# Performance work log

Hardware: AMD Instinct MI355X
Metric: run time of the kernel (lower is better)

Reference implementation:

```python
import jax, jax.numpy as jnp
import numpy as np
from jax import lax

THRESHOLD = 0.7
OUT = 224  # output size of nn.Upsample(size=(224,224), mode='bilinear', align_corners=True)


def _bilinear(img, xs, ys):
    """align_corners=True bilinear sampling. img: (..., H, W); xs: (oh,), ys: (ow,) float coords."""
    H, W = img.shape[-2], img.shape[-1]
    x0 = jnp.clip(jnp.floor(xs).astype(jnp.int32), 0, H - 1)
    x1 = jnp.clip(x0 + 1, 0, H - 1)
    y0 = jnp.clip(jnp.floor(ys).astype(jnp.int32), 0, W - 1)
    y1 = jnp.clip(y0 + 1, 0, W - 1)
    wx = (xs - x0.astype(xs.dtype))[:, None]  # (oh,1)
    wy = (ys - y0.astype(ys.dtype))[None, :]  # (1,ow)
    top = jnp.take(img, x0, axis=-2)
    bot = jnp.take(img, x1, axis=-2)
    v00 = jnp.take(top, y0, axis=-1)
    v01 = jnp.take(top, y1, axis=-1)
    v10 = jnp.take(bot, y0, axis=-1)
    v11 = jnp.take(bot, y1, axis=-1)
    return (1 - wx) * ((1 - wy) * v00 + wy * v01) + wx * ((1 - wy) * v10 + wy * v11)


def _normalize01(h):
    n = h.shape[0]
    f = h.reshape(n, -1)
    mn = f.min(axis=1, keepdims=True)
    mx = f.max(axis=1, keepdims=True)
    return ((f - mn) / (mx - mn)).reshape(h.shape)


def _largest_cc(mask):
    """8-connected (skimage connectivity=2) largest component via min-label propagation.
    mask: (N,H,W) bool -> (N,H,W) bool, True on the largest connected component."""
    N, H, W = mask.shape
    BIG = H * W  # background sentinel label
    idx = jnp.arange(BIG, dtype=jnp.int32).reshape(1, H, W)
    lab0 = jnp.where(mask, idx, BIG)

    def body(state):
        lab, _ = state
        pooled = lax.reduce_window(lab, jnp.int32(BIG), lax.min, (1, 3, 3), (1, 1, 1), 'SAME')
        new = jnp.where(mask, pooled, BIG)
        return new, jnp.any(new != lab)

    lab, _ = lax.while_loop(lambda s: s[1], body, (lab0, jnp.bool_(True)))

    def counts(l):
        return jnp.zeros(BIG + 1, jnp.int32).at[l.reshape(-1)].add(1)

    c = jax.vmap(counts)(lab)                 # (N, H*W+1); last bin = background
    best = jnp.argmax(c[:, :BIG], axis=1)     # label of largest foreground component
    return lab == best[:, None, None]


def _bbox(lcc):
    N, H, W = lcc.shape
    rows = lcc.any(axis=2)
    cols = lcc.any(axis=1)
    has = rows.any(axis=1)
    xmin = jnp.argmax(rows, axis=1).astype(jnp.int32)
    xmax = (H - 1 - jnp.argmax(rows[:, ::-1], axis=1)).astype(jnp.int32)
    ymin = jnp.argmax(cols, axis=1).astype(jnp.int32)
    ymax = (W - 1 - jnp.argmax(cols[:, ::-1], axis=1)).astype(jnp.int32)
    # fallback to full image if the mask is empty (torch code would crash here)
    xmin = jnp.where(has, xmin, 0)
    ymin = jnp.where(has, ymin, 0)
    xmax = jnp.where(has, xmax, H - 1)
    ymax = jnp.where(has, ymax, W - 1)
    return xmin, xmax, ymin, ymax


def _crop_resize(images, xmin, xmax, ymin, ymax):
    # torch crop is images[i][:, xmin:xmax, ymin:ymax] (exclusive upper), then align_corners resize
    grid = jnp.arange(OUT, dtype=jnp.float32) / (OUT - 1)

    def one(img, a, b, c, d):
        Lx = jnp.maximum(b - a, 1)
        Ly = jnp.maximum(d - c, 1)
        xs = a.astype(jnp.float32) + grid * (Lx - 1).astype(jnp.float32)
        ys = c.astype(jnp.float32) + grid * (Ly - 1).astype(jnp.float32)
        return _bilinear(img, xs, ys)

    return jax.vmap(one)(images, xmin, xmax, ymin, ymax)


def setup_inputs() -> dict:
    key = jax.random.key(0)
    k1, k2 = jax.random.split(key)
    x = jax.random.normal(k1, (64, 3, 224, 224), dtype=jnp.float32)
    features = jax.random.normal(k2, (64, 2048, 7, 7), dtype=jnp.float32)
    return {"x": x, "features": features}


def reference(x, features):
    # distance = normalize01(Lmax(features, axis=1))
    heat = _normalize01(jnp.max(jnp.abs(features), axis=1))       # (N, h, w)
    h, w = heat.shape[1], heat.shape[2]
    grid = jnp.arange(OUT, dtype=jnp.float32) / (OUT - 1)
    out_heatmap = _bilinear(heat, grid * (h - 1), grid * (w - 1))  # (N, 224, 224)
    mask = out_heatmap > THRESHOLD
    lcc = _largest_cc(mask)
    xmin, xmax, ymin, ymax = _bbox(lcc)
    crop = _crop_resize(x, xmin, xmax, ymin, ymax)                 # (N, 3, 224, 224)
    coords = jnp.stack([ymin, xmin, ymax, xmax], axis=1)           # (N, 4), torch coord order
    return crop, out_heatmap, coords
```

## Files before the change

kernel.cpp:

```cpp
#include <hip/hip_runtime.h>
#include <stdint.h>

#define NIMG   64
#define NCH    2048
#define HW7    49
#define OUTW   224
#define NPIX   50176
#define CROP_N 9633792
#define HEAT_OFF  9633792
#define COORD_OFF 12845056
#define THRESH 0.7f

#define MAXR 4
#define RCAP (224*MAXR)
#define NWORDS 784
#define WPAD   788

#define NGRP 16


__global__ __launch_bounds__(256) void k1_heat(const float* __restrict__ F,
                                               float* __restrict__ heatPart) {
    __shared__ float smax[4][64];
    const int t = threadIdx.x;
    const int b = blockIdx.x;
    const int n = b >> 4, g = b & 15;
    const int w = t >> 6, l = t & 63;
    const int lp = (l < HW7) ? l : 0;
    const float* base = F + (size_t)n * 100352 + (size_t)(g * 128 + w) * HW7 + lp;
    float vmax = 0.0f;
#pragma unroll 8
    for (int i = 0; i < 32; ++i) {
        vmax = fmaxf(vmax, fabsf(base[(size_t)i * 4 * HW7]));
    }
    smax[w][l] = vmax;
    __syncthreads();
    if (t < HW7) {
        float m = fmaxf(fmaxf(smax[0][t], smax[1][t]), fmaxf(smax[2][t], smax[3][t]));
        heatPart[b * HW7 + t] = m;
    }
}

__device__ inline unsigned uf_find(volatile unsigned* P, unsigned x) {
    while (true) {
        unsigned p = P[x];
        if (p == x) return x;
        unsigned gp = P[p];
        if (gp == p) return p;
        P[x] = gp;
        x = gp;
    }
}

__device__ inline void uf_merge(volatile unsigned* P, unsigned a, unsigned b) {
    while (true) {
        a = uf_find(P, a); b = uf_find(P, b);
        if (a == b) return;
        if (a > b) { unsigned tmp = a; a = b; b = tmp; }
        unsigned old = atomicCAS((unsigned*)&P[b], b, a);
        if (old == b) return;
        b = old;
    }
}

__global__ __launch_bounds__(1024) void k23_heat_ccl(const float* __restrict__ heatPart,
                                                     float* __restrict__ heatOut,
                                                     float* __restrict__ coords) {
#pragma clang fp contract(off)
    __shared__ float raw[HW7];
    __shared__ float h7[HW7];
    __shared__ float s_mn, s_mx;
    __shared__ float wT[OUTW];
    __shared__ int   i0T[OUTW];
    __shared__ int   i1T[OUTW];
    __shared__ unsigned long long W[WPAD];
    __shared__ unsigned short runS[RCAP], runE[RCAP];
    __shared__ unsigned char nRuns[224];
    __shared__ unsigned parent[RCAP], cnt[RCAP];
    __shared__ unsigned rmin[RCAP], rmax[RCAP], cmin[RCAP], cmax[RCAP];
    __shared__ unsigned bestScore, bestRid;

    const int t = threadIdx.x;
    const int n = blockIdx.x;

    if (t < HW7) {
        float m = heatPart[(n * NGRP + 0) * HW7 + t];
#pragma unroll
        for (int g = 1; g < NGRP; ++g) m = fmaxf(m, heatPart[(n * NGRP + g) * HW7 + t]);
        raw[t] = m;
    }
    if (t < OUTW) {
        float gx = (float)t / 223.0f;
        float xs = gx * 6.0f;
        int x0 = (int)floorf(xs); x0 = min(max(x0, 0), 6);
        i0T[t] = x0;
        i1T[t] = min(x0 + 1, 6);
        wT[t]  = xs - (float)x0;
    }
    if (t < RCAP) {
        parent[t] = (unsigned)t; cnt[t] = 0u;
        rmin[t] = 0xFFFFFFFFu; rmax[t] = 0u; cmin[t] = 0xFFFFFFFFu; cmax[t] = 0u;
    }
    if (t >= NWORDS && t < WPAD) W[t] = 0ull;
    if (t == 0) { bestScore = 0u; bestRid = 0u; }
    __syncthreads();
    if (t == 0) {
        float mn = raw[0], mx = raw[0];
        for (int i = 1; i < HW7; ++i) { float v = raw[i]; mn = fminf(mn, v); mx = fmaxf(mx, v); }
        s_mn = mn; s_mx = mx;
    }
    __syncthreads();
    if (t < HW7) h7[t] = (raw[t] - s_mn) / (s_mx - s_mn);
    __syncthreads();

    for (int k = 0; k < 49; ++k) {
        int p = (k << 10) + t;
        int i = p / 224, j = p - i * 224;
        int x0 = i0T[i], x1 = i1T[i];
        int y0 = i0T[j], y1 = i1T[j];
        float wx = wT[i], wy = wT[j];
        float v00 = h7[x0 * 7 + y0], v01 = h7[x0 * 7 + y1];
        float v10 = h7[x1 * 7 + y0], v11 = h7[x1 * 7 + y1];
        float val = (1.0f - wx) * ((1.0f - wy) * v00 + wy * v01)
                  + wx * ((1.0f - wy) * v10 + wy * v11);
        heatOut[(size_t)n * NPIX + p] = val;
        unsigned long long bal = __ballot(val > THRESH);
        if ((t & 63) == 0) W[p >> 6] = bal;
    }
    __syncthreads();

    if (t < 224) {
        const int r = t;
        const int bit0 = r * 224;
        const int w0 = bit0 >> 6, sh = bit0 & 63;
        unsigned long long rb[4];
#pragma unroll
        for (int q = 0; q < 4; ++q) {
            unsigned long long lo = W[w0 + q] >> sh;
            unsigned long long hi = sh ? (W[w0 + q + 1] << (64 - sh)) : 0ull;
            rb[q] = lo | hi;
        }
        rb[3] &= 0xFFFFFFFFull;

        unsigned long long st[4], en[4];
        unsigned long long carry = 0ull;
#pragma unroll
        for (int q = 0; q < 4; ++q) {
            unsigned long long shl = (rb[q] << 1) | carry;
            carry = rb[q] >> 63;
            st[q] = rb[q] & ~shl;
        }
#pragma unroll
        for (int q = 0; q < 4; ++q) {
            unsigned long long nxt = (q < 3) ? rb[q + 1] : 0ull;
            en[q] = rb[q] & ~((rb[q] >> 1) | (nxt << 63));
        }
        int ns = 0;
#pragma unroll
        for (int q = 0; q < 4; ++q) {
            unsigned long long x = st[q];
            while (x) {
                int z = __builtin_ctzll(x); x &= x - 1;
                if (ns < MAXR) runS[r * MAXR + ns] = (unsigned short)(q * 64 + z);
                ns++;
            }
        }
        int ne = 0;
#pragma unroll
        for (int q = 0; q < 4; ++q) {
            unsigned long long x = en[q];
            while (x) {
                int z = __builtin_ctzll(x); x &= x - 1;
                if (ne < MAXR) runE[r * MAXR + ne] = (unsigned short)(q * 64 + z);
                ne++;
            }
        }
        nRuns[r] = (unsigned char)min(ns, MAXR);
    }
    __syncthreads();

    if (t >= MAXR && t < RCAP) {
        const int r = t >> 2, k = t & (MAXR - 1);
        if (k < (int)nRuns[r]) {
            const int nb = nRuns[r - 1];
            int s = runS[t], e = runE[t];
            for (int m = 0; m < nb; ++m) {
                int qid = (r - 1) * MAXR + m;
                int s2 = runS[qid], e2 = runE[qid];
                if (s2 <= e + 1 && e2 >= s - 1) uf_merge(parent, (unsigned)t, (unsigned)qid);
            }
        }
    }
    __syncthreads();

    if (t < RCAP) {
        int r = t >> 2, k = t & (MAXR - 1);
        if (k < (int)nRuns[r]) {
            int s = runS[t], e = runE[t];
            unsigned root = uf_find(parent, (unsigned)t);
            atomicAdd(&cnt[root], (unsigned)(e - s + 1));
            atomicMin(&rmin[root], (unsigned)r);
            atomicMax(&rmax[root], (unsigned)r);
            atomicMin(&cmin[root], (unsigned)s);
            atomicMax(&cmax[root], (unsigned)e);
        }
    }
    __syncthreads();

    if (t < RCAP) {
        unsigned c = cnt[t];
        if (c > 0u) {
            unsigned label = (unsigned)((t >> 2) * 224 + (int)runS[t]);
            unsigned score = (c << 16) | (65535u - label);
            atomicMax(&bestScore, score);
        }
    }
    __syncthreads();
    if (t < RCAP) {
        unsigned c = cnt[t];
        if (c > 0u) {
            unsigned label = (unsigned)((t >> 2) * 224 + (int)runS[t]);
            unsigned score = (c << 16) | (65535u - label);
            if (score == bestScore) bestRid = (unsigned)t;
        }
    }
    __syncthreads();

    if (t == 0) {
        int xmin, xmax, ymin, ymax;
        if (bestScore == 0u) {
            xmin = 0; ymin = 0; xmax = 223; ymax = 223;
        } else {
            unsigned rb_ = bestRid;
            xmin = (int)rmin[rb_]; xmax = (int)rmax[rb_];
            ymin = (int)cmin[rb_]; ymax = (int)cmax[rb_];
        }
        coords[n * 4 + 0] = (float)ymin;
        coords[n * 4 + 1] = (float)xmin;
        coords[n * 4 + 2] = (float)ymax;
        coords[n * 4 + 3] = (float)xmax;
    }
}

__global__ __launch_bounds__(256) void k4_crop(const float* __restrict__ X,
                                               const float* __restrict__ coords,
                                               float* __restrict__ out) {
#pragma clang fp contract(off)
    const int t = threadIdx.x;
    const int b = blockIdx.x;
    const int n = b / 49;
    const int p4 = ((b % 49) * 256 + t) * 4;
    const int oi = p4 / 224, oj = p4 - oi * 224;

    int ymin = (int)coords[n * 4 + 0];
    int xmin = (int)coords[n * 4 + 1];
    int ymax = (int)coords[n * 4 + 2];
    int xmax = (int)coords[n * 4 + 3];
    int Lx = max(xmax - xmin, 1);
    int Ly = max(ymax - ymin, 1);

    float gx = (float)oi / 223.0f;
    float xs = (float)xmin + gx * (float)(Lx - 1);
    int x0 = (int)floorf(xs); x0 = min(max(x0, 0), 223); int x1 = min(x0 + 1, 223);
    float wx = xs - (float)x0;

    int   y0q[4], y1q[4];
    float wyq[4];
#pragma unroll
    for (int q = 0; q < 4; ++q) {
        float gy = (float)(oj + q) / 223.0f;
        float ys = (float)ymin + gy * (float)(Ly - 1);
        int y0 = (int)floorf(ys); y0 = min(max(y0, 0), 223);
        y0q[q] = y0; y1q[q] = min(y0 + 1, 223);
        wyq[q] = ys - (float)y0;
    }

    const float* img = X + (size_t)n * 150528;
    float* obase = out + (size_t)n * 150528 + p4;
#pragma unroll
    for (int ch = 0; ch < 3; ++ch) {
        const float* rt = img + ch * NPIX + x0 * 224;
        const float* rb = img + ch * NPIX + x1 * 224;
        float r[4];
#pragma unroll
        for (int q = 0; q < 4; ++q) {
            float v00 = rt[y0q[q]], v01 = rt[y1q[q]];
            float v10 = rb[y0q[q]], v11 = rb[y1q[q]];
            r[q] = (1.0f - wx) * ((1.0f - wyq[q]) * v00 + wyq[q] * v01)
                 + wx * ((1.0f - wyq[q]) * v10 + wyq[q] * v11);
        }
        *reinterpret_cast<float4*>(obase + (size_t)ch * NPIX) =
            make_float4(r[0], r[1], r[2], r[3]);
    }
}

extern "C" void kernel_launch(void* const* d_in, const int* in_sizes, int n_in,
                              void* d_out, int out_size, void* d_ws, size_t ws_size,
                              hipStream_t stream) {
    (void)in_sizes; (void)n_in; (void)out_size; (void)d_ws; (void)ws_size;
    const float* X = (const float*)d_in[0];
    const float* F = (const float*)d_in[1];
    float* out = (float*)d_out;

    float* heatPart = (float*)d_out;
    float* heatOut = out + HEAT_OFF;
    float* coords  = out + COORD_OFF;

    k1_heat     <<<dim3(1024), dim3(256),  0, stream>>>(F, heatPart);
    k23_heat_ccl<<<dim3(64),   dim3(1024), 0, stream>>>(heatPart, heatOut, coords);
    k4_crop     <<<dim3(3136), dim3(256),  0, stream>>>(X, coords, out);
}
```

Baseline: 143.2 us.

## Split heatmap upsample across two blocks per image with last-block CCL

The heatmap upsampling and mask generation for each image is now split across two 1024-thread blocks, doubling the grid to 128 blocks. Each block writes its mask words to a global scratch area inside the output buffer. A per-image atomic counter lets the last-arriving block reload the full mask and run the connected-component and bbox stage alone. This trades extra global traffic and an atomic handoff for more parallelism in the heatmap write phase on a GPU that was mostly idle with 64 blocks.

```diff
diff --git a/kernel.cpp b/kernel.cpp
--- a/kernel.cpp
+++ b/kernel.cpp
@@ -18,12 +18,18 @@
 
 #define NGRP 16
 
+#define MASKW_BYTE_OFF 262144
+#define CNT_BYTE_OFF   663552
 
 __global__ __launch_bounds__(256) void k1_heat(const float* __restrict__ F,
-                                               float* __restrict__ heatPart) {
+                                               float* __restrict__ heatPart,
+                                               unsigned* __restrict__ imgCnt) {
     __shared__ float smax[4][64];
     const int t = threadIdx.x;
     const int b = blockIdx.x;
+    if (b == 0 && t < NIMG) {
+        __hip_atomic_store(&imgCnt[t], 0u, __ATOMIC_RELAXED, __HIP_MEMORY_SCOPE_AGENT);
+    }
     const int n = b >> 4, g = b & 15;
     const int w = t >> 6, l = t & 63;
     const int lp = (l < HW7) ? l : 0;
@@ -63,8 +69,10 @@
     }
 }
 
-__global__ __launch_bounds__(1024) void k23_heat_ccl(const float* __restrict__ heatPart,
+__global__ __launch_bounds__(1024) void k23_heatmask(const float* __restrict__ heatPart,
                                                      float* __restrict__ heatOut,
+                                                     unsigned long long* __restrict__ maskW,
+                                                     unsigned* __restrict__ imgCnt,
                                                      float* __restrict__ coords) {
 #pragma clang fp contract(off)
     __shared__ float raw[HW7];
@@ -73,6 +81,7 @@
     __shared__ float wT[OUTW];
     __shared__ int   i0T[OUTW];
     __shared__ int   i1T[OUTW];
+    __shared__ int   s_last;
     __shared__ unsigned long long W[WPAD];
     __shared__ unsigned short runS[RCAP], runE[RCAP];
     __shared__ unsigned char nRuns[224];
@@ -81,7 +90,8 @@
     __shared__ unsigned bestScore, bestRid;
 
     const int t = threadIdx.x;
-    const int n = blockIdx.x;
+    const int b = blockIdx.x;
+    const int n = b >> 1, slice = b & 1;
 
     if (t < HW7) {
         float m = heatPart[(n * NGRP + 0) * HW7 + t];
@@ -97,12 +107,6 @@
         i1T[t] = min(x0 + 1, 6);
         wT[t]  = xs - (float)x0;
     }
-    if (t < RCAP) {
-        parent[t] = (unsigned)t; cnt[t] = 0u;
-        rmin[t] = 0xFFFFFFFFu; rmax[t] = 0u; cmin[t] = 0xFFFFFFFFu; cmax[t] = 0u;
-    }
-    if (t >= NWORDS && t < WPAD) W[t] = 0ull;
-    if (t == 0) { bestScore = 0u; bestRid = 0u; }
     __syncthreads();
     if (t == 0) {
         float mn = raw[0], mx = raw[0];
@@ -113,20 +117,45 @@
     if (t < HW7) h7[t] = (raw[t] - s_mn) / (s_mx - s_mn);
     __syncthreads();
 
-    for (int k = 0; k < 49; ++k) {
-        int p = (k << 10) + t;
-        int i = p / 224, j = p - i * 224;
-        int x0 = i0T[i], x1 = i1T[i];
-        int y0 = i0T[j], y1 = i1T[j];
-        float wx = wT[i], wy = wT[j];
-        float v00 = h7[x0 * 7 + y0], v01 = h7[x0 * 7 + y1];
-        float v10 = h7[x1 * 7 + y0], v11 = h7[x1 * 7 + y1];
-        float val = (1.0f - wx) * ((1.0f - wy) * v00 + wy * v01)
-                  + wx * ((1.0f - wy) * v10 + wy * v11);
-        heatOut[(size_t)n * NPIX + p] = val;
-        unsigned long long bal = __ballot(val > THRESH);
-        if ((t & 63) == 0) W[p >> 6] = bal;
-    }
+    const int pbase = slice * 25088;
+    for (int k = 0; k < 25; ++k) {
+        int pl = (k << 10) + t;
+        if (pl < 25088) {
+            int p = pbase + pl;
+            int i = p / 224, j = p - i * 224;
+            int x0 = i0T[i], x1 = i1T[i];
+            int y0 = i0T[j], y1 = i1T[j];
+            float wx = wT[i], wy = wT[j];
+            float v00 = h7[x0 * 7 + y0], v01 = h7[x0 * 7 + y1];
+            float v10 = h7[x1 * 7 + y0], v11 = h7[x1 * 7 + y1];
+            float val = (1.0f - wx) * ((1.0f - wy) * v00 + wy * v01)
+                      + wx * ((1.0f - wy) * v10 + wy * v11);
+            heatOut[(size_t)n * NPIX + p] = val;
+            unsigned long long bal = __ballot(val > THRESH);
+            if ((t & 63) == 0) {
+                __hip_atomic_store(&maskW[(size_t)n * NWORDS + (p >> 6)], bal,
+                                   __ATOMIC_RELAXED, __HIP_MEMORY_SCOPE_AGENT);
+            }
+        }
+    }
+
+    __syncthreads();
+    if (t == 0) {
+        unsigned old = __hip_atomic_fetch_add(&imgCnt[n], 1u,
+                                              __ATOMIC_ACQ_REL, __HIP_MEMORY_SCOPE_AGENT);
+        s_last = (old == 1u);
+    }
+    __syncthreads();
+    if (!s_last) return;
+
+    if (t < NWORDS) W[t] = __hip_atomic_load(&maskW[(size_t)n * NWORDS + t],
+                                             __ATOMIC_RELAXED, __HIP_MEMORY_SCOPE_AGENT);
+    if (t >= NWORDS && t < WPAD) W[t] = 0ull;
+    if (t < RCAP) {
+        parent[t] = (unsigned)t; cnt[t] = 0u;
+        rmin[t] = 0xFFFFFFFFu; rmax[t] = 0u; cmin[t] = 0xFFFFFFFFu; cmax[t] = 0u;
+    }
+    if (t == 0) { bestScore = 0u; bestRid = 0u; }
     __syncthreads();
 
     if (t < 224) {
@@ -303,10 +332,12 @@
     float* out = (float*)d_out;
 
     float* heatPart = (float*)d_out;
+    unsigned long long* maskW = (unsigned long long*)((char*)d_out + MASKW_BYTE_OFF);
+    unsigned* imgCnt = (unsigned*)((char*)d_out + CNT_BYTE_OFF);
     float* heatOut = out + HEAT_OFF;
     float* coords  = out + COORD_OFF;
 
-    k1_heat     <<<dim3(1024), dim3(256),  0, stream>>>(F, heatPart);
-    k23_heat_ccl<<<dim3(64),   dim3(1024), 0, stream>>>(heatPart, heatOut, coords);
+    k1_heat     <<<dim3(1024), dim3(256),  0, stream>>>(F, heatPart, imgCnt);
+    k23_heatmask<<<dim3(128),  dim3(1024), 0, stream>>>(heatPart, heatOut, maskW, imgCnt, coords);
     k4_crop     <<<dim3(3136), dim3(256),  0, stream>>>(X, coords, out);
 }
```

Result: faster. 138.3 us (median of 2 runs) (-3.4%).
